# Performance work log

Hardware: AMD Instinct MI355X
Metric: run time of the kernel (lower is better)

## Reference

```python
import jax, jax.numpy as jnp
import numpy as np

N_ENTITY = 100000
N_RELATION = 64
DIM = 16
N_HOP = 2
N_MEM = 32
N_NODES = 16384


def setup_inputs() -> dict:
    key = jax.random.key(0)
    ks = jax.random.split(key, 7)
    return {
        "nodes": jax.random.randint(ks[0], (N_NODES,), 0, N_ENTITY),
        "memories_h": jax.random.randint(ks[1], (N_HOP, N_NODES, N_MEM), 0, N_ENTITY),
        "memories_r": jax.random.randint(ks[2], (N_HOP, N_NODES, N_MEM), 0, N_RELATION),
        "memories_t": jax.random.randint(ks[3], (N_HOP, N_NODES, N_MEM), 0, N_ENTITY),
        "entity_emb": jax.random.normal(ks[4], (N_ENTITY, DIM), jnp.float32) * 0.1,
        "relation_emb": jax.random.normal(ks[5], (N_RELATION, DIM * DIM), jnp.float32) * 0.1,
        "W": jax.random.normal(ks[6], (DIM, DIM), jnp.float32) * 0.1,
    }


def reference(nodes, memories_h, memories_r, memories_t, entity_emb, relation_emb, W):
    # item embeddings for the query nodes: [N, D]
    item = entity_emb[nodes]
    o_list = []
    for hop in range(N_HOP):  # small fixed hop count (2)
        h = entity_emb[memories_h[hop]]                                  # [N, M, D]
        r = relation_emb[memories_r[hop]].reshape(-1, N_MEM, DIM, DIM)   # [N, M, D, D]
        t = entity_emb[memories_t[hop]]                                  # [N, M, D]
        # Rh = R @ h : [N, M, D]
        Rh = jnp.einsum('nmde,nme->nmd', r, h)
        # attention over the n_memory slots (softmax dim=0 per node in original)
        probs = jax.nn.softmax(jnp.einsum('nmd,nd->nm', Rh, item), axis=1)
        # weighted sum of tails: [N, D]
        o = jnp.einsum('nm,nmd->nd', probs, t)
        # item_update_mode == 'plus_transform': Linear(dim, dim, bias=False)
        item = (item + o) @ W.T
        o_list.append(o)
    # Faithful to the original torch in-place semantics: at hop 0 the line
    # `kg_feature += o_list[0]` doubles o0 in place; the final result for
    # n_hop=2 is therefore o1 + 2*o0.
    return o_list[1] + 2.0 * o_list[0]
```

## Files before the change

### kernel.cpp

```cpp
#include <hip/hip_runtime.h>

#define NE     100000
#define NR     64
#define DIM    16
#define NHOP   2
#define NMEM   32
#define NNODES 16384

#define WPITCH 20
#define ET_BYTES (NE * DIM * 2)
#define NB_ET  ((NE * DIM / 4 + 255) / 256)

typedef __attribute__((ext_vector_type(2))) _Float16 half2_t;

static __device__ __forceinline__ half2_t as_h2(unsigned u) {
    union { unsigned i; half2_t h; } c; c.i = u; return c.h;
}
static __device__ __forceinline__ float qdot2(unsigned u, unsigned ip, float q) {
#if __has_builtin(__builtin_amdgcn_fdot2)
    return __builtin_amdgcn_fdot2(as_h2(u), as_h2(ip), q, false);
#else
    half2_t a = as_h2(u), b = as_h2(ip);
    return q + (float)a.x * (float)b.x + (float)a.y * (float)b.y;
#endif
}
static __device__ __forceinline__ float dpp_sum16(float v) {
    union { int i; float f; } a, b;
    a.f = v;
    b.i = __builtin_amdgcn_update_dpp(0, a.i, 0xB1,  0xf, 0xf, true); a.f += b.f;
    b.i = __builtin_amdgcn_update_dpp(0, a.i, 0x4E,  0xf, 0xf, true); a.f += b.f;
    b.i = __builtin_amdgcn_update_dpp(0, a.i, 0x124, 0xf, 0xf, true); a.f += b.f;
    b.i = __builtin_amdgcn_update_dpp(0, a.i, 0x128, 0xf, 0xf, true); a.f += b.f;
    return a.f;
}
static __device__ __forceinline__ float bcast(float v, int l) {
    return __int_as_float(__builtin_amdgcn_readlane(__float_as_int(v), l));
}
static __device__ __forceinline__ unsigned short f2h(float f) {
    union { _Float16 h; unsigned short s; } c; c.h = (_Float16)f; return c.s;
}
static __device__ __forceinline__ unsigned pack2h(float a, float b) {
    union { _Float16 h[2]; unsigned u; } c;
    c.h[0] = (_Float16)a; c.h[1] = (_Float16)b;
    return c.u;
}

extern "C" __global__ void __launch_bounds__(256)
prep_kernel(const float* __restrict__ ent, const float* __restrict__ rel,
            _Float16* __restrict__ et, unsigned short* __restrict__ rtg, int n4)
{
    const int b = blockIdx.x, tid = threadIdx.x;
    if (b < NB_ET) {
        int i = b * 256 + tid;
        if (i < n4) {
            float4 v = ((const float4*)ent)[i];
            union { _Float16 h[4]; unsigned long long u; } c;
            c.h[0] = (_Float16)v.x; c.h[1] = (_Float16)v.y;
            c.h[2] = (_Float16)v.z; c.h[3] = (_Float16)v.w;
            *(unsigned long long*)(et + 4 * (long long)i) = c.u;
        }
    } else {
        int j = (b - NB_ET) * 256 + tid;
        const float4* rel4 = (const float4*)rel;
        #pragma unroll
        for (int k = 0; k < 4; ++k) {
            int vidx = k * 1024 + j;
            float4 v = rel4[vidx];
            int k0 = vidx * 4;
            int r  = k0 >> 8;
            int kk = k0 & 255;
            int d  = kk >> 4;
            int e0 = kk & 15;
            int phys = ((d >> 2) + (e0 >> 2)) & 3;
            unsigned short* p = &rtg[r * 256 + e0 * 16 + phys * 4 + (d & 3)];
            p[0]  = f2h(v.x);
            p[16] = f2h(v.y);
            p[32] = f2h(v.z);
            p[48] = f2h(v.w);
        }
    }
}

extern "C" __global__ void __launch_bounds__(256, 4)
ripple_kernel(const int* __restrict__ nodes,
              const int* __restrict__ mh,
              const int* __restrict__ mr,
              const int* __restrict__ mt,
              const _Float16* __restrict__ et,
              const unsigned short* __restrict__ rtg,
              const float* __restrict__ W,
              float* __restrict__ out)
{
    __shared__ __align__(16) unsigned short rt[NR * 256];
    __shared__ __align__(16) float ws[DIM * WPITCH];

    const int tid  = threadIdx.x;
    const int lane = tid & 63;
    const int wid  = tid >> 6;
    const int g    = lane >> 4;
    const int e    = lane & 15;
    const int n    = blockIdx.x * 4 + wid;

    const int ib0 = 0 * (NNODES * NMEM) + n * NMEM + g * 8;
    const int ib1 = 1 * (NNODES * NMEM) + n * NMEM + g * 8;
    int hi0[8], ri0[8], ti0[8], hi1[8], ri1[8], ti1[8];
    {
        const int4* p;
        p = (const int4*)(mh + ib0); *(int4*)&hi0[0] = p[0]; *(int4*)&hi0[4] = p[1];
        p = (const int4*)(mr + ib0); *(int4*)&ri0[0] = p[0]; *(int4*)&ri0[4] = p[1];
        p = (const int4*)(mt + ib0); *(int4*)&ti0[0] = p[0]; *(int4*)&ti0[4] = p[1];
        p = (const int4*)(mh + ib1); *(int4*)&hi1[0] = p[0]; *(int4*)&hi1[4] = p[1];
        p = (const int4*)(mr + ib1); *(int4*)&ri1[0] = p[0]; *(int4*)&ri1[4] = p[1];
        p = (const int4*)(mt + ib1); *(int4*)&ti1[0] = p[0]; *(int4*)&ti1[4] = p[1];
    }
    const int nd = nodes[n];

    float4 stg[8];
    {
        const float4* src = (const float4*)rtg;
        #pragma unroll
        for (int i = 0; i < 8; ++i) stg[i] = src[i * 256 + tid];
    }
    const float wv = W[tid];

    float item = (float)et[nd * DIM + e];
    float hv0[8], tv0[8], hv1[8], tv1[8];
    #pragma unroll
    for (int it = 0; it < 8; ++it) {
        hv0[it] = (float)et[hi0[it] * DIM + e];
        tv0[it] = (float)et[ti0[it] * DIM + e];
        hv1[it] = (float)et[hi1[it] * DIM + e];
        tv1[it] = (float)et[ti1[it] * DIM + e];
    }

    {
        float4* dst = (float4*)rt;
        #pragma unroll
        for (int i = 0; i < 8; ++i) dst[i * 256 + tid] = stg[i];
        ws[(tid >> 4) * WPITCH + (tid & 15)] = wv;
    }
    __syncthreads();

    int voff[4];
    {
        const int s = e >> 2;
        #pragma unroll
        for (int j = 0; j < 4; ++j)
            voff[j] = e * 32 + (((j + s) & 3) << 3);
    }

    float out_acc = 0.f;

    #pragma unroll
    for (int hop = 0; hop < NHOP; ++hop) {
        const int*   ri = hop ? ri1 : ri0;
        const float* hv = hop ? hv1 : hv0;
        const float* tv = hop ? tv1 : tv0;

        unsigned ip[8];
        #pragma unroll
        for (int j = 0; j < 8; ++j)
            ip[j] = pack2h(bcast(item, 2 * j), bcast(item, 2 * j + 1));

        float Z = 0.f, o = 0.f;
        #pragma unroll
        for (int it = 0; it < 8; ++it) {
            const char* rbase = (const char*)rt + (ri[it] << 9);
            float q = 0.f;
            #pragma unroll
            for (int j = 0; j < 4; ++j) {
                uint2 u = *(const uint2*)(rbase + voff[j]);
                q = qdot2(u.x, ip[2 * j + 0], q);
                q = qdot2(u.y, ip[2 * j + 1], q);
            }
            float sc = dpp_sum16(q * hv[it]);
            float ex = __expf(sc);
            Z += ex;
            o += ex * tv[it];
        }
        Z += __shfl_xor(Z, 16);
        Z += __shfl_xor(Z, 32);
        o += __shfl_xor(o, 16);
        o += __shfl_xor(o, 32);
        o *= 1.f / Z;

        out_acc += (hop == 0) ? 2.f * o : o;

        const float v = item + o;
        float nit = 0.f;
        const float4* wr = (const float4*)&ws[e * WPITCH];
        #pragma unroll
        for (int j = 0; j < 4; ++j) {
            float4 w = wr[j];
            nit += w.x * bcast(v, 4 * j + 0) + w.y * bcast(v, 4 * j + 1)
                 + w.z * bcast(v, 4 * j + 2) + w.w * bcast(v, 4 * j + 3);
        }
        item = nit;
    }

    if (lane < 16) out[n * DIM + e] = out_acc;
}

extern "C" void kernel_launch(void* const* d_in, const int* in_sizes, int n_in,
                              void* d_out, int out_size, void* d_ws, size_t ws_size,
                              hipStream_t stream) {
    const int*   nodes = (const int*)d_in[0];
    const int*   mh    = (const int*)d_in[1];
    const int*   mr    = (const int*)d_in[2];
    const int*   mt    = (const int*)d_in[3];
    const float* ent   = (const float*)d_in[4];
    const float* rel   = (const float*)d_in[5];
    const float* W     = (const float*)d_in[6];
    float*       out   = (float*)d_out;

    _Float16*       et  = (_Float16*)d_ws;
    unsigned short* rtg = (unsigned short*)((char*)d_ws + ET_BYTES);

    const int n4 = NE * DIM / 4;
    prep_kernel<<<NB_ET + 4, 256, 0, stream>>>(ent, rel, et, rtg, n4);

    dim3 grid(NNODES / 4);
    dim3 block(256);
    ripple_kernel<<<grid, block, 0, stream>>>(nodes, mh, mr, mt, et, rtg, W, out);
}
```

Baseline: 101.2 us.

## Fuse fp16 prep into main kernel and double block size to 512 threads

Removes the separate prep kernel that converted the whole entity table to fp16 and re-laid out the relation matrices. The main kernel now gathers fp32 entity rows directly and builds the swizzled fp16 relation table in shared memory from the fp32 source on every block. Blocks grow to 8 waves (512 threads) so the per-block relation staging cost is spread over twice as many nodes. This drops a launch and a full-table conversion pass, but each gather now moves twice the bytes, and every block does strided fp32 reads of the relation tensor.

```diff
diff --git a/kernel.cpp b/kernel.cpp
--- a/kernel.cpp
+++ b/kernel.cpp
@@ -8,8 +8,6 @@
 #define NNODES 16384
 
 #define WPITCH 20
-#define ET_BYTES (NE * DIM * 2)
-#define NB_ET  ((NE * DIM / 4 + 255) / 256)
 
 typedef __attribute__((ext_vector_type(2))) _Float16 half2_t;
 
@@ -36,58 +34,19 @@
 static __device__ __forceinline__ float bcast(float v, int l) {
     return __int_as_float(__builtin_amdgcn_readlane(__float_as_int(v), l));
 }
-static __device__ __forceinline__ unsigned short f2h(float f) {
-    union { _Float16 h; unsigned short s; } c; c.h = (_Float16)f; return c.s;
-}
 static __device__ __forceinline__ unsigned pack2h(float a, float b) {
     union { _Float16 h[2]; unsigned u; } c;
     c.h[0] = (_Float16)a; c.h[1] = (_Float16)b;
     return c.u;
 }
 
-extern "C" __global__ void __launch_bounds__(256)
-prep_kernel(const float* __restrict__ ent, const float* __restrict__ rel,
-            _Float16* __restrict__ et, unsigned short* __restrict__ rtg, int n4)
-{
-    const int b = blockIdx.x, tid = threadIdx.x;
-    if (b < NB_ET) {
-        int i = b * 256 + tid;
-        if (i < n4) {
-            float4 v = ((const float4*)ent)[i];
-            union { _Float16 h[4]; unsigned long long u; } c;
-            c.h[0] = (_Float16)v.x; c.h[1] = (_Float16)v.y;
-            c.h[2] = (_Float16)v.z; c.h[3] = (_Float16)v.w;
-            *(unsigned long long*)(et + 4 * (long long)i) = c.u;
-        }
-    } else {
-        int j = (b - NB_ET) * 256 + tid;
-        const float4* rel4 = (const float4*)rel;
-        #pragma unroll
-        for (int k = 0; k < 4; ++k) {
-            int vidx = k * 1024 + j;
-            float4 v = rel4[vidx];
-            int k0 = vidx * 4;
-            int r  = k0 >> 8;
-            int kk = k0 & 255;
-            int d  = kk >> 4;
-            int e0 = kk & 15;
-            int phys = ((d >> 2) + (e0 >> 2)) & 3;
-            unsigned short* p = &rtg[r * 256 + e0 * 16 + phys * 4 + (d & 3)];
-            p[0]  = f2h(v.x);
-            p[16] = f2h(v.y);
-            p[32] = f2h(v.z);
-            p[48] = f2h(v.w);
-        }
-    }
-}
-
-extern "C" __global__ void __launch_bounds__(256, 4)
+extern "C" __global__ void __launch_bounds__(512, 4)
 ripple_kernel(const int* __restrict__ nodes,
               const int* __restrict__ mh,
               const int* __restrict__ mr,
               const int* __restrict__ mt,
-              const _Float16* __restrict__ et,
-              const unsigned short* __restrict__ rtg,
+              const float* __restrict__ ent,
+              const float* __restrict__ rel,
               const float* __restrict__ W,
               float* __restrict__ out)
 {
@@ -99,7 +58,7 @@
     const int wid  = tid >> 6;
     const int g    = lane >> 4;
     const int e    = lane & 15;
-    const int n    = blockIdx.x * 4 + wid;
+    const int n    = blockIdx.x * 8 + wid;
 
     const int ib0 = 0 * (NNODES * NMEM) + n * NMEM + g * 8;
     const int ib1 = 1 * (NNODES * NMEM) + n * NMEM + g * 8;
@@ -115,30 +74,34 @@
     }
     const int nd = nodes[n];
 
-    float4 stg[8];
     {
-        const float4* src = (const float4*)rtg;
         #pragma unroll
-        for (int i = 0; i < 8; ++i) stg[i] = src[i * 256 + tid];
+        for (int it = 0; it < 8; ++it) {
+            const int idx = it * 512 + tid;
+            const int e0  = idx & 15;
+            const int dq  = (idx >> 4) & 3;
+            const int r   = idx >> 6;
+            const float* s = rel + r * 256 + dq * 64 + e0;
+            const float f0 = s[0], f1 = s[16], f2 = s[32], f3 = s[48];
+            const int phys = (dq + (e0 >> 2)) & 3;
+            uint2 pk;
+            pk.x = pack2h(f0, f1);
+            pk.y = pack2h(f2, f3);
+            *(uint2*)((char*)rt + (r << 9) + (e0 << 5) + (phys << 3)) = pk;
+        }
+        if (tid < 256) ws[(tid >> 4) * WPITCH + (tid & 15)] = W[tid];
     }
-    const float wv = W[tid];
 
-    float item = (float)et[nd * DIM + e];
+    float item = ent[nd * DIM + e];
     float hv0[8], tv0[8], hv1[8], tv1[8];
     #pragma unroll
     for (int it = 0; it < 8; ++it) {
-        hv0[it] = (float)et[hi0[it] * DIM + e];
-        tv0[it] = (float)et[ti0[it] * DIM + e];
-        hv1[it] = (float)et[hi1[it] * DIM + e];
-        tv1[it] = (float)et[ti1[it] * DIM + e];
+        hv0[it] = ent[hi0[it] * DIM + e];
+        tv0[it] = ent[ti0[it] * DIM + e];
+        hv1[it] = ent[hi1[it] * DIM + e];
+        tv1[it] = ent[ti1[it] * DIM + e];
     }
 
-    {
-        float4* dst = (float4*)rt;
-        #pragma unroll
-        for (int i = 0; i < 8; ++i) dst[i * 256 + tid] = stg[i];
-        ws[(tid >> 4) * WPITCH + (tid & 15)] = wv;
-    }
     __syncthreads();
 
     int voff[4];
@@ -213,13 +176,9 @@
     const float* W     = (const float*)d_in[6];
     float*       out   = (float*)d_out;
 
-    _Float16*       et  = (_Float16*)d_ws;
-    unsigned short* rtg = (unsigned short*)((char*)d_ws + ET_BYTES);
+    (void)d_ws; (void)ws_size;
 
-    const int n4 = NE * DIM / 4;
-    prep_kernel<<<NB_ET + 4, 256, 0, stream>>>(ent, rel, et, rtg, n4);
-
-    dim3 grid(NNODES / 4);
-    dim3 block(256);
-    ripple_kernel<<<grid, block, 0, stream>>>(nodes, mh, mr, mt, et, rtg, W, out);
+    dim3 grid(NNODES / 8);
+    dim3 block(512);
+    ripple_kernel<<<grid, block, 0, stream>>>(nodes, mh, mr, mt, ent, rel, W, out);
 }
```

After: 105.9 us. +4.6%, slower.
